# Kernel optimization log

Hardware: AMD Instinct MI355X
Metric: run time of the kernel (lower is better)

The kernel has to match this reference:

```python
import jax, jax.numpy as jnp
import numpy as np

N = 100_000          # nodes
E = 1_600_000        # edges (avg degree 16)
N_GRAPHS = 64        # batched graphs for sum_nodes readout
SLOPE_ATTN = 0.2     # leaky_relu slope on attention logits (GAT standard)
SLOPE_INTER = 0.01   # F.leaky_relu default between layers


def _gat_layer(xn, xe, src, dst, Wn, bn, Wv, bv, We, be, a_s, a_e, a_d, a_b, num_nodes):
    # Multi-head GAT with edge features. Wn:[H,Din,Dz] attn proj, Wv:[H,Din,Do] value proj,
    # We:[H,Ein,De] edge proj. Attention logit = a_s.z_src + a_e.ze + a_d.z_dst + b
    # (equivalent to attn_fc(cat(z_src, ze, z_dst)) without materializing the concat).
    z = jnp.einsum('nd,hdk->nhk', xn, Wn) + bn            # [N,H,Dz]
    v = jnp.einsum('nd,hdk->nhk', xn, Wv) + bv            # [N,H,Do]
    ze = jnp.einsum('ed,hdk->ehk', xe, We) + be           # [E,H,De]
    s = (jnp.einsum('ehk,hk->eh', z[src], a_s)
         + jnp.einsum('ehk,hk->eh', ze, a_e)
         + jnp.einsum('ehk,hk->eh', z[dst], a_d) + a_b)   # [E,H]
    s = jax.nn.leaky_relu(s, SLOPE_ATTN)
    # edge-softmax grouped by destination node (stable)
    m = jax.ops.segment_max(s, dst, num_segments=num_nodes)
    m = jnp.where(jnp.isfinite(m), m, 0.0)
    ex = jnp.exp(s - m[dst])
    den = jax.ops.segment_sum(ex, dst, num_segments=num_nodes)
    alpha = ex / (den[dst] + 1e-9)                        # [E,H]
    h = jax.ops.segment_sum(alpha[..., None] * v[src], dst, num_segments=num_nodes)  # [N,H,Do]
    Eh, H, De = ze.shape
    return h.reshape(num_nodes, -1), ze.reshape(Eh, H * De)


def setup_inputs() -> dict:
    key = jax.random.key(0)
    ks = jax.random.split(key, 32)
    f = lambda i, shape: jax.random.normal(ks[i], shape, dtype=jnp.float32) * 0.1
    return dict(
        node_types=f(0, (N, 14)),
        node_labels=f(1, (N, 50)),
        edge_labels=f(2, (E, 32)),
        src=jax.random.randint(ks[3], (E,), 0, N),
        dst=jax.random.randint(ks[4], (E,), 0, N),
        graph_ids=jnp.sort(jax.random.randint(ks[5], (N,), 0, N_GRAPHS)),
        l0_Wn=f(6, (2, 64, 32)), l0_bn=f(7, (2, 32)),
        l0_Wv=f(8, (2, 64, 64)), l0_bv=f(9, (2, 64)),
        l0_We=f(10, (2, 32, 16)), l0_be=f(11, (2, 16)),
        l0_as=f(12, (2, 32)), l0_ae=f(13, (2, 16)), l0_ad=f(14, (2, 32)), l0_ab=f(15, (2,)),
        l1_Wn=f(16, (2, 128, 32)), l1_bn=f(17, (2, 32)),
        l1_Wv=f(18, (2, 128, 64)), l1_bv=f(19, (2, 64)),
        l1_We=f(20, (2, 32, 16)), l1_be=f(21, (2, 16)),
        l1_as=f(22, (2, 32)), l1_ae=f(23, (2, 16)), l1_ad=f(24, (2, 32)), l1_ab=f(25, (2,)),
        fc_W=f(26, (128, 2)), fc_b=f(27, (2,)),
    )


def reference(node_types, node_labels, edge_labels, src, dst, graph_ids,
              l0_Wn, l0_bn, l0_Wv, l0_bv, l0_We, l0_be, l0_as, l0_ae, l0_ad, l0_ab,
              l1_Wn, l1_bn, l1_Wv, l1_bv, l1_We, l1_be, l1_as, l1_ae, l1_ad, l1_ab,
              fc_W, fc_b):
    xn = jnp.concatenate([node_types, node_labels], axis=1)   # node_features_use == 'all'
    xe = edge_labels
    xn, xe = _gat_layer(xn, xe, src, dst, l0_Wn, l0_bn, l0_Wv, l0_bv,
                        l0_We, l0_be, l0_as, l0_ae, l0_ad, l0_ab, N)
    xn = jax.nn.leaky_relu(xn, SLOPE_INTER)
    xe = jax.nn.leaky_relu(xe, SLOPE_INTER)
    xn, xe = _gat_layer(xn, xe, src, dst, l1_Wn, l1_bn, l1_Wv, l1_bv,
                        l1_We, l1_be, l1_as, l1_ae, l1_ad, l1_ab, N)
    # dgl.sum_nodes over batched graphs, then classification FC
    graph_sum = jax.ops.segment_sum(xn, graph_ids, num_segments=N_GRAPHS)  # [G, 128]
    return graph_sum @ fc_W + fc_b
```

## Files before the change

### kernel.cpp

```cpp
#include <hip/hip_runtime.h>

#define NN 100000
#define EE 1600000
#define NG 64

#define BSH 9
#define NWIN 512
#define NB 196
#define CAP 10240
#define EPB 4096

#define OFF_WS0 0
#define OFF_WD0 128
#define OFF_CS0 256
#define OFF_CD0 258
#define OFF_U1  260
#define OFF_C1  324
#define OFF_WS1 512
#define OFF_WD1 768
#define OFF_CS1 1024
#define OFF_CD1 1026
#define OFF_WT0 2048
#define FOLD_FLOATS 4096

typedef __attribute__((ext_vector_type(8))) short short8;
typedef __attribute__((ext_vector_type(4))) float f32x4;

__device__ __forceinline__ unsigned encm(float f) {
  unsigned u = __float_as_uint(f);
  return (u & 0x80000000u) ? ~u : (u | 0x80000000u);
}
__device__ __forceinline__ float decm(unsigned u) {
  return (u & 0x80000000u) ? __uint_as_float(u & 0x7FFFFFFFu) : __uint_as_float(~u);
}
__device__ __forceinline__ unsigned bf16r(float f) {
  unsigned u = __float_as_uint(f);
  return (u + 0x7FFFu + ((u >> 16) & 1u)) >> 16;
}

__global__ void fold_k(const float* __restrict__ Wn0, const float* __restrict__ bn0,
                       const float* __restrict__ as0, const float* __restrict__ ad0,
                       const float* __restrict__ We0,
                       const float* __restrict__ We1, const float* __restrict__ be1,
                       const float* __restrict__ ae1,
                       const float* __restrict__ Wn1, const float* __restrict__ bn1,
                       const float* __restrict__ as1, const float* __restrict__ ad1,
                       const float* __restrict__ Wv1,
                       float* __restrict__ fold, unsigned* __restrict__ w1tw) {
  int t = threadIdx.x;
  for (int i = t; i < 128; i += 256) {
    int h = i >> 6, d = i & 63;
    float s = 0.f, sd = 0.f;
    for (int k = 0; k < 32; ++k) {
      float w = Wn0[h*2048 + d*32 + k];
      s  += w * as0[h*32 + k];
      sd += w * ad0[h*32 + k];
    }
    fold[OFF_WS0 + i] = s; fold[OFF_WD0 + i] = sd;
  }
  for (int i = t; i < 64; i += 256) {
    int h = i >> 5, d = i & 31;
    float s = 0.f;
    for (int k = 0; k < 16; ++k) s += We1[h*512 + d*16 + k] * ae1[h*16 + k];
    fold[OFF_U1 + i] = s;
  }
  for (int i = t; i < 1024; i += 256) {
    int o = i >> 5, d = i & 31;
    fold[OFF_WT0 + o*32 + d] = We0[(o >> 4)*512 + d*16 + (o & 15)];
  }
  for (int i = t; i < 8192; i += 256) {
    int o = i >> 6, dw = i & 63;
    int d0 = 2*dw, d1 = d0 + 1;
    float f0 = Wv1[(o >> 6)*8192 + d0*64 + (o & 63)];
    float f1 = Wv1[(o >> 6)*8192 + d1*64 + (o & 63)];
    w1tw[i] = bf16r(f0) | (bf16r(f1) << 16);
  }
  if (t < 256) {
    int i = t, h = i >> 7, d = i & 127;
    float s = 0.f, sd = 0.f;
    for (int k = 0; k < 32; ++k) {
      float w = Wn1[h*4096 + d*32 + k];
      s  += w * as1[h*32 + k];
      sd += w * ad1[h*32 + k];
    }
    fold[OFF_WS1 + i] = s; fold[OFF_WD1 + i] = sd;
  }
  if (t < 2) {
    float cs = 0.f, cd = 0.f;
    for (int k = 0; k < 32; ++k) { cs += bn0[t*32+k]*as0[t*32+k]; cd += bn0[t*32+k]*ad0[t*32+k]; }
    fold[OFF_CS0 + t] = cs; fold[OFF_CD0 + t] = cd;
    float c1 = 0.f;
    for (int k = 0; k < 16; ++k) c1 += ae1[t*16+k]*be1[t*16+k];
    fold[OFF_C1 + t] = c1;
    float cs1 = 0.f, cd1 = 0.f;
    for (int k = 0; k < 32; ++k) { cs1 += bn1[t*32+k]*as1[t*32+k]; cd1 += bn1[t*32+k]*ad1[t*32+k]; }
    fold[OFF_CS1 + t] = cs1; fold[OFF_CD1 + t] = cd1;
  }
}

__global__ __launch_bounds__(256) void binA_k(const int* __restrict__ dst,
                                              int* __restrict__ bcur, uint2* __restrict__ stg) {
  __shared__ int hist[NB], gbase[NB];
  int tid = threadIdx.x;
  for (int i = tid; i < NB; i += 256) hist[i] = 0;
  __syncthreads();
  int e0 = blockIdx.x*EPB;
  int dd[16], li[16];
  #pragma unroll
  for (int q = 0; q < 16; ++q) {
    int e = e0 + q*256 + tid;
    if (e < EE) {
      int dn = dst[e];
      dd[q] = dn;
      li[q] = atomicAdd(&hist[dn >> BSH], 1);
    }
  }
  __syncthreads();
  if (tid < NB) gbase[tid] = atomicAdd(&bcur[tid], hist[tid]);
  __syncthreads();
  #pragma unroll
  for (int q = 0; q < 16; ++q) {
    int e = e0 + q*256 + tid;
    if (e < EE) {
      int b = dd[q] >> BSH;
      int idx = gbase[b] + li[q];
      if (idx < CAP) stg[(size_t)b*CAP + idx] = make_uint2((unsigned)e, (unsigned)dd[q]);
    }
  }
}

__global__ void scanB_k(const int* __restrict__ bcur, int* __restrict__ bbase) {
  int s = 0;
  for (int b = 0; b < NB; ++b) { bbase[b] = s; s += bcur[b]; }
}

__global__ __launch_bounds__(256) void binB_k(const uint2* __restrict__ stg, const int* __restrict__ bcur,
                                              const int* __restrict__ bbase,
                                              int* __restrict__ off, int* __restrict__ eid,
                                              int* __restrict__ dnp) {
  __shared__ int hist[NWIN], curx[NWIN], wsum[4];
  int tid = threadIdx.x, lane = tid & 63, w = tid >> 6;
  int b = blockIdx.x;
  int nbase = b << BSH;
  int cnt = bcur[b], base = bbase[b];
  for (int i = tid; i < NWIN; i += 256) hist[i] = 0;
  __syncthreads();
  const uint2* sp = stg + (size_t)b*CAP;
  for (int i = tid; i < cnt; i += 256) atomicAdd(&hist[sp[i].y - nbase], 1);
  __syncthreads();
  int a0 = hist[2*tid], a1 = hist[2*tid + 1];
  int tsum = a0 + a1;
  int x = tsum;
  #pragma unroll
  for (int o = 1; o < 64; o <<= 1) { int y = __shfl_up(x, o); if (lane >= o) x += y; }
  if (lane == 63) wsum[w] = x;
  __syncthreads();
  if (tid == 0) { int s = 0; for (int q = 0; q < 4; ++q) { int t = wsum[q]; wsum[q] = s; s += t; } }
  __syncthreads();
  int excl = wsum[w] + x - tsum;
  curx[2*tid]     = base + excl;
  curx[2*tid + 1] = base + excl + a0;
  __syncthreads();
  for (int j = tid; j < NWIN; j += 256) {
    int n = nbase + j;
    if (n < NN) off[n] = curx[j];
  }
  if (b == NB - 1 && tid == 0) off[NN] = base + cnt;
  __syncthreads();
  for (int i = tid; i < cnt; i += 256) {
    uint2 r = sp[i];
    int p = atomicAdd(&curx[r.y - nbase], 1);
    eid[p] = (int)r.x;
    dnp[p] = (int)r.y;
  }
}

__global__ __launch_bounds__(128) void node0v_k(const float* __restrict__ nt, const float* __restrict__ nl,
                                                const float* __restrict__ Wv0, const float* __restrict__ bv0,
                                                unsigned* __restrict__ v0b) {
  int tid = threadIdx.x;
  int h = tid >> 6, k = tid & 63;
  int sl2 = k & 31;
  float w[64];
  #pragma unroll
  for (int d = 0; d < 64; ++d) w[d] = Wv0[h*4096 + d*64 + k];
  float b = bv0[tid];
  int nb = blockIdx.x * 8;
  #pragma unroll 1
  for (int r = 0; r < 8; ++r) {
    int n = nb + r;
    const float* nrow = nt + (size_t)n*14;
    const float* lrow = nl + (size_t)n*50;
    float acc = b;
    #pragma unroll
    for (int d = 0; d < 14; ++d) acc = fmaf(nrow[d], w[d], acc);
    #pragma unroll
    for (int d = 0; d < 50; ++d) acc = fmaf(lrow[d], w[14 + d], acc);
    float p0 = __shfl(acc, 2*sl2);
    float p1 = __shfl(acc, 2*sl2 + 1);
    if (k < 32) v0b[(size_t)n*64 + h*32 + sl2] = bf16r(p0) | (bf16r(p1) << 16);
  }
}

__global__ __launch_bounds__(256) void nodez_k(const float* __restrict__ nt, const float* __restrict__ nl,
                                               const float* __restrict__ fold,
                                               float* __restrict__ zs0, float* __restrict__ zd0) {
  int n = blockIdx.x*256 + threadIdx.x;
  if (n >= NN) return;
  float p0 = 0.f, p1 = 0.f, p2 = 0.f, p3 = 0.f;
  #pragma unroll
  for (int d = 0; d < 64; ++d) {
    float x = (d < 14) ? nt[(size_t)n*14 + d] : nl[(size_t)n*50 + d - 14];
    p0 = fmaf(x, fold[OFF_WS0 + d],      p0);
    p1 = fmaf(x, fold[OFF_WS0 + 64 + d], p1);
    p2 = fmaf(x, fold[OFF_WD0 + d],      p2);
    p3 = fmaf(x, fold[OFF_WD0 + 64 + d], p3);
  }
  zs0[n*2]   = p0 + fold[OFF_CS0];
  zs0[n*2+1] = p1 + fold[OFF_CS0+1];
  zd0[n*2]   = p2 + fold[OFF_CD0];
  zd0[n*2+1] = p3 + fold[OFF_CD0+1];
}

__global__ __launch_bounds__(256) void edge0_k(const float* __restrict__ xe,
                                               const int* __restrict__ src,
                                               const int* __restrict__ eid, const int* __restrict__ dnp,
                                               const float* __restrict__ be0,
                                               const float* __restrict__ ae0, const float* __restrict__ ab0,
                                               const float* __restrict__ fold,
                                               const float* __restrict__ zs0, const float* __restrict__ zd0,
                                               float4* __restrict__ ebuf, float* __restrict__ et1p,
                                               int* __restrict__ snp,
                                               unsigned* __restrict__ menc0, unsigned* __restrict__ menc1) {
  int p = blockIdx.x*256 + threadIdx.x;
  int lane = threadIdx.x & 63;
  int e = eid[p];
  int dn = dnp[p];
  int sn = src[e];
  const float4* xp = reinterpret_cast<const float4*>(xe + (size_t)e*32);
  float4 xv[8];
  #pragma unroll
  for (int q = 0; q < 8; ++q) xv[q] = xp[q];
  const float* WT = fold + OFF_WT0;
  const float* U1 = fold + OFF_U1;
  float s0 = 0.f, s1 = 0.f, etA = 0.f, etB = 0.f;
  #pragma unroll 4
  for (int o = 0; o < 16; ++o) {
    float acc = be0[o];
    #pragma unroll
    for (int q = 0; q < 8; ++q) {
      float4 w = *reinterpret_cast<const float4*>(WT + o*32 + q*4);
      acc = fmaf(xv[q].x, w.x, acc); acc = fmaf(xv[q].y, w.y, acc);
      acc = fmaf(xv[q].z, w.z, acc); acc = fmaf(xv[q].w, w.w, acc);
    }
    s0 = fmaf(ae0[o], acc, s0);
    float lz = acc >= 0.f ? acc : 0.01f*acc;
    etA = fmaf(lz, U1[o], etA); etB = fmaf(lz, U1[32 + o], etB);
  }
  #pragma unroll 4
  for (int o = 16; o < 32; ++o) {
    float acc = be0[o];
    #pragma unroll
    for (int q = 0; q < 8; ++q) {
      float4 w = *reinterpret_cast<const float4*>(WT + o*32 + q*4);
      acc = fmaf(xv[q].x, w.x, acc); acc = fmaf(xv[q].y, w.y, acc);
      acc = fmaf(xv[q].z, w.z, acc); acc = fmaf(xv[q].w, w.w, acc);
    }
    s1 = fmaf(ae0[o], acc, s1);
    float lz = acc >= 0.f ? acc : 0.01f*acc;
    etA = fmaf(lz, U1[o], etA); etB = fmaf(lz, U1[32 + o], etB);
  }
  float2 zsv = *reinterpret_cast<const float2*>(zs0 + (size_t)sn*2);
  float2 zdv = *reinterpret_cast<const float2*>(zd0 + (size_t)dn*2);
  float l0 = zsv.x + s0 + zdv.x + ab0[0];
  float l1 = zsv.y + s1 + zdv.y + ab0[1];
  l0 = l0 >= 0.f ? l0 : 0.2f*l0;
  l1 = l1 >= 0.f ? l1 : 0.2f*l1;
  float etA1 = etA + fold[OFF_C1], etB1 = etB + fold[OFF_C1+1];
  ebuf[p] = make_float4(__int_as_float(sn), l0, l1, 0.f);
  *reinterpret_cast<float2*>(et1p + (size_t)p*2) = make_float2(etA1, etB1);
  snp[p] = sn;
  unsigned e0 = encm(l0), e1 = encm(l1), e2 = encm(etA1), e3 = encm(etB1);
  #pragma unroll
  for (int o = 1; o < 64; o <<= 1) {
    int pdn = __shfl_down(dn, o);
    unsigned q0 = __shfl_down(e0, o);
    unsigned q1 = __shfl_down(e1, o);
    unsigned q2 = __shfl_down(e2, o);
    unsigned q3 = __shfl_down(e3, o);
    if (pdn == dn) { e0 = max(e0, q0); e1 = max(e1, q1); e2 = max(e2, q2); e3 = max(e3, q3); }
  }
  int prev = __shfl_up(dn, 1);
  if (lane == 0 || prev != dn) {
    atomicMax(&menc0[(size_t)dn*2],   e0);
    atomicMax(&menc0[(size_t)dn*2+1], e1);
    atomicMax(&menc1[(size_t)dn*2],   e2);
    atomicMax(&menc1[(size_t)dn*2+1], e3);
  }
}

__global__ __launch_bounds__(256) void agg0_k(const int* __restrict__ off,
                                              const float4* __restrict__ ebuf,
                                              const unsigned* __restrict__ menc,
                                              const unsigned* __restrict__ v0b,
                                              const float* __restrict__ fold,
                                              unsigned* __restrict__ xb,
                                              float* __restrict__ zs1, float* __restrict__ zd1) {
  int tid = threadIdx.x, w = tid >> 6, lane = tid & 63;
  int n = blockIdx.x*4 + w;
  int head = lane >> 5;
  int st = off[n], en = off[n+1];
  float m = decm(menc[(size_t)n*2 + head]);
  float alo = 0.f, ahi = 0.f, den = 0.f;
  for (int i = st; i < en; i += 8) {
    int nv = en - i;
    float4 eb[8]; unsigned vr[8];
    #pragma unroll
    for (int q = 0; q < 8; ++q) if (q < nv) eb[q] = ebuf[i + q];
    #pragma unroll
    for (int q = 0; q < 8; ++q) if (q < nv) vr[q] = v0b[(size_t)__float_as_int(eb[q].x)*64 + lane];
    #pragma unroll
    for (int q = 0; q < 8; ++q) {
      if (q < nv) {
        float s = head ? eb[q].z : eb[q].y;
        float e = __expf(s - m);
        den += e;
        alo = fmaf(e, __uint_as_float(vr[q] << 16),         alo);
        ahi = fmaf(e, __uint_as_float(vr[q] & 0xFFFF0000u), ahi);
      }
    }
  }
  float inv = 1.f / (den + 1e-9f);
  float xlo = alo*inv, xhi = ahi*inv;
  xlo = xlo >= 0.f ? xlo : 0.01f*xlo;
  xhi = xhi >= 0.f ? xhi : 0.01f*xhi;
  xb[(size_t)n*64 + lane] = bf16r(xlo) | (bf16r(xhi) << 16);
  const float2* ws1 = reinterpret_cast<const float2*>(fold + OFF_WS1);
  const float2* wd1 = reinterpret_cast<const float2*>(fold + OFF_WD1);
  float2 wa = ws1[lane], wb = ws1[64 + lane], wc = wd1[lane], wd = wd1[64 + lane];
  float p0 = xlo*wa.x + xhi*wa.y;
  float p1 = xlo*wb.x + xhi*wb.y;
  float p2 = xlo*wc.x + xhi*wc.y;
  float p3 = xlo*wd.x + xhi*wd.y;
  #pragma unroll
  for (int o = 32; o > 0; o >>= 1) {
    p0 += __shfl_down(p0, o); p1 += __shfl_down(p1, o);
    p2 += __shfl_down(p2, o); p3 += __shfl_down(p3, o);
  }
  if (lane == 0) {
    zs1[n*2]   = p0 + fold[OFF_CS1];
    zs1[n*2+1] = p1 + fold[OFF_CS1+1];
    zd1[n*2]   = p2 + fold[OFF_CD1];
    zd1[n*2+1] = p3 + fold[OFF_CD1+1];
  }
}

__global__ __launch_bounds__(256) void zmax_k(const float* __restrict__ zs1, unsigned* __restrict__ zmaxenc) {
  int n = blockIdx.x*256 + threadIdx.x;
  int lane = threadIdx.x & 63;
  unsigned e0 = 0u, e1 = 0u;
  if (n < NN) {
    e0 = encm(zs1[(size_t)n*2]);
    e1 = encm(zs1[(size_t)n*2 + 1]);
  }
  #pragma unroll
  for (int o = 32; o > 0; o >>= 1) {
    e0 = max(e0, (unsigned)__shfl_down(e0, o));
    e1 = max(e1, (unsigned)__shfl_down(e1, o));
  }
  if (lane == 0) {
    atomicMax(&zmaxenc[0], e0);
    atomicMax(&zmaxenc[1], e1);
  }
}

__global__ __launch_bounds__(256) void node1m_k(const unsigned* __restrict__ xb,
                                                const unsigned* __restrict__ w1tw,
                                                const float* __restrict__ bv1,
                                                unsigned short* __restrict__ v1s) {
  int tid = threadIdx.x, w = tid >> 6, lane = tid & 63;
  int tile = blockIdx.x*4 + w;
  if (tile >= NN/16) return;
  int row = lane & 15, kg = lane >> 4;
  int n = tile*16 + row;
  short8 a[4];
  #pragma unroll
  for (int ks = 0; ks < 4; ++ks)
    a[ks] = *reinterpret_cast<const short8*>(xb + (size_t)n*64 + ks*16 + kg*4);
  #pragma unroll 2
  for (int t = 0; t < 8; ++t) {
    float bias = bv1[t*16 + row];
    f32x4 acc = {bias, bias, bias, bias};
    #pragma unroll
    for (int ks = 0; ks < 4; ++ks) {
      short8 b = *reinterpret_cast<const short8*>(w1tw + (size_t)(t*16 + row)*64 + ks*16 + kg*4);
      acc = __builtin_amdgcn_mfma_f32_16x16x32_bf16(a[ks], b, acc, 0, 0, 0);
    }
    int o = t*16 + row;
    #pragma unroll
    for (int r = 0; r < 4; ++r) {
      int nr = tile*16 + kg*4 + r;
      v1s[(size_t)nr*128 + o] = (unsigned short)bf16r(acc[r]);
    }
  }
}

__global__ void outinit_k(const float* __restrict__ fcb, float* __restrict__ out) {
  int i = threadIdx.x;
  out[i] = fcb[i & 1];
}

__global__ __launch_bounds__(256) void agg1_k(const int* __restrict__ off,
                                              const int* __restrict__ snp,
                                              const float* __restrict__ et1p,
                                              const float* __restrict__ zs1, const float* __restrict__ zd1,
                                              const float* __restrict__ ab1,
                                              const unsigned* __restrict__ menc1,
                                              const unsigned* __restrict__ zmaxenc,
                                              const unsigned* __restrict__ v1b,
                                              const float* __restrict__ fcW,
                                              float* __restrict__ pnode) {
  int tid = threadIdx.x, w = tid >> 6, lane = tid & 63;
  int n = blockIdx.x*4 + w;
  int head = lane >> 5;
  int st = off[n], en = off[n+1];
  float cnode = zd1[(size_t)n*2 + head] + ab1[head];
  float B = decm(menc1[(size_t)n*2 + head]) + decm(zmaxenc[head]) + cnode;
  float m = B >= 0.f ? B : 0.2f*B;
  float alo = 0.f, ahi = 0.f, den = 0.f;
  for (int i = st; i < en; i += 8) {
    int nv = en - i;
    int sn[8]; float et[8]; unsigned vr[8]; float zr[8];
    #pragma unroll
    for (int q = 0; q < 8; ++q) {
      if (q < nv) {
        sn[q] = snp[i + q];
        et[q] = et1p[(size_t)(i + q)*2 + head];
      }
    }
    #pragma unroll
    for (int q = 0; q < 8; ++q) {
      if (q < nv) {
        vr[q] = v1b[(size_t)sn[q]*64 + lane];
        zr[q] = zs1[(size_t)sn[q]*2 + head];
      }
    }
    #pragma unroll
    for (int q = 0; q < 8; ++q) {
      if (q < nv) {
        float l = zr[q] + et[q] + cnode;
        l = l >= 0.f ? l : 0.2f*l;
        float e = __expf(l - m);
        den += e;
        alo = fmaf(e, __uint_as_float(vr[q] << 16),         alo);
        ahi = fmaf(e, __uint_as_float(vr[q] & 0xFFFF0000u), ahi);
      }
    }
  }
  float inv = 1.f / (den + 1e-9f);
  float hlo = alo*inv, hhi = ahi*inv;
  const float2* fw2 = reinterpret_cast<const float2*>(fcW);
  float2 f0 = fw2[2*lane], f1 = fw2[2*lane + 1];
  float p0 = hlo*f0.x + hhi*f1.x;
  float p1 = hlo*f0.y + hhi*f1.y;
  #pragma unroll
  for (int o = 32; o > 0; o >>= 1) {
    p0 += __shfl_down(p0, o);
    p1 += __shfl_down(p1, o);
  }
  if (lane == 0) {
    pnode[n*2]   = p0;
    pnode[n*2+1] = p1;
  }
}

__global__ __launch_bounds__(256) void gsum_k(const float* __restrict__ pnode, const int* __restrict__ gid,
                                              float* __restrict__ out) {
  int n = blockIdx.x*256 + threadIdx.x;
  int lane = threadIdx.x & 63;
  bool ok = n < NN;
  int g = ok ? gid[n] : -1;
  float p0 = ok ? pnode[n*2]   : 0.f;
  float p1 = ok ? pnode[n*2+1] : 0.f;
  #pragma unroll
  for (int o = 1; o < 64; o <<= 1) {
    int pg = __shfl_down(g, o);
    float q0 = __shfl_down(p0, o);
    float q1 = __shfl_down(p1, o);
    if ((lane + o) < 64 && pg == g) { p0 += q0; p1 += q1; }
  }
  int prev = __shfl_up(g, 1);
  if (ok && (lane == 0 || prev != g)) {
    atomicAdd(&out[g*2],     p0);
    atomicAdd(&out[g*2 + 1], p1);
  }
}

extern "C" void kernel_launch(void* const* d_in, const int* in_sizes, int n_in,
                              void* d_out, int out_size, void* d_ws, size_t ws_size,
                              hipStream_t stream) {
  const float* nt  = (const float*)d_in[0];
  const float* nl  = (const float*)d_in[1];
  const float* xe  = (const float*)d_in[2];
  const int*   src = (const int*)d_in[3];
  const int*   dst = (const int*)d_in[4];
  const int*   gid = (const int*)d_in[5];
  const float* Wn0 = (const float*)d_in[6],  *bn0 = (const float*)d_in[7];
  const float* Wv0 = (const float*)d_in[8],  *bv0 = (const float*)d_in[9];
  const float* We0 = (const float*)d_in[10], *be0 = (const float*)d_in[11];
  const float* as0 = (const float*)d_in[12], *ae0 = (const float*)d_in[13];
  const float* ad0 = (const float*)d_in[14], *ab0 = (const float*)d_in[15];
  const float* Wn1 = (const float*)d_in[16], *bn1 = (const float*)d_in[17];
  const float* Wv1 = (const float*)d_in[18], *bv1 = (const float*)d_in[19];
  const float* We1 = (const float*)d_in[20], *be1 = (const float*)d_in[21];
  const float* as1 = (const float*)d_in[22], *ae1 = (const float*)d_in[23];
  const float* ad1 = (const float*)d_in[24], *ab1 = (const float*)d_in[25];
  const float* fcW = (const float*)d_in[26], *fcb = (const float*)d_in[27];
  float* out = (float*)d_out;

  float* fold  = (float*)d_ws;
  float* zs    = fold + FOLD_FLOATS;
  float* zd    = zs + (size_t)NN*2;
  unsigned* v0b = (unsigned*)(zd + (size_t)NN*2);
  unsigned* v1b = v0b + (size_t)NN*64;
  unsigned* xb  = v1b + (size_t)NN*64;
  unsigned* w1tw = xb + (size_t)NN*64;
  float* et1p  = (float*)(w1tw + 128*64);
  float* ebuff = et1p + (size_t)EE*2;
  unsigned* menc0 = (unsigned*)(ebuff + (size_t)EE*4);
  unsigned* menc1 = menc0 + (size_t)NN*2;
  unsigned* zmaxenc = menc1 + (size_t)NN*2;
  int* bcur   = (int*)(zmaxenc + 2);
  int* bbase  = bcur + NB;
  float* pnode = (float*)(bbase + NB);
  int* off    = (int*)(pnode + (size_t)NN*2);
  int* eid    = off + NN + 1;
  int* dnp    = eid + EE;
  int* snp    = dnp + EE;
  uint2* stg  = (uint2*)(snp + EE);
  float4* ebuf = (float4*)ebuff;

  hipMemsetAsync(menc0, 0, ((size_t)NN*4 + 2 + NB)*sizeof(unsigned), stream);
  fold_k<<<1, 256, 0, stream>>>(Wn0, bn0, as0, ad0, We0, We1, be1, ae1, Wn1, bn1, as1, ad1, Wv1, fold, w1tw);
  binA_k<<<(EE + EPB - 1)/EPB, 256, 0, stream>>>(dst, bcur, stg);
  scanB_k<<<1, 1, 0, stream>>>(bcur, bbase);
  binB_k<<<NB, 256, 0, stream>>>(stg, bcur, bbase, off, eid, dnp);
  node0v_k<<<NN/8, 128, 0, stream>>>(nt, nl, Wv0, bv0, v0b);
  nodez_k<<<(NN + 255)/256, 256, 0, stream>>>(nt, nl, fold, zs, zd);
  edge0_k<<<EE/256, 256, 0, stream>>>(xe, src, eid, dnp, be0, ae0, ab0, fold, zs, zd,
                                      ebuf, et1p, snp, menc0, menc1);
  agg0_k<<<NN/4, 256, 0, stream>>>(off, ebuf, menc0, v0b, fold, xb, zs, zd);
  zmax_k<<<(NN + 255)/256, 256, 0, stream>>>(zs, zmaxenc);
  node1m_k<<<(NN/16 + 3)/4, 256, 0, stream>>>(xb, w1tw, bv1, (unsigned short*)v1b);
  outinit_k<<<1, 128, 0, stream>>>(fcb, out);
  agg1_k<<<NN/4, 256, 0, stream>>>(off, snp, et1p, zs, zd, ab1, menc1, zmaxenc, v1b, fcW, pnode);
  gsum_k<<<(NN + 255)/256, 256, 0, stream>>>(pnode, gid, out);
}
```

Measured before the change: 589.4 us.

## Shrink edge buffer to float2 logits, reuse snp, deepen aggregation batches

```diff
diff --git a/kernel.cpp b/kernel.cpp
--- a/kernel.cpp
+++ b/kernel.cpp
@@ -229,7 +229,7 @@
                                                const float* __restrict__ ae0, const float* __restrict__ ab0,
                                                const float* __restrict__ fold,
                                                const float* __restrict__ zs0, const float* __restrict__ zd0,
-                                               float4* __restrict__ ebuf, float* __restrict__ et1p,
+                                               float* __restrict__ sbuf, float* __restrict__ et1p,
                                                int* __restrict__ snp,
                                                unsigned* __restrict__ menc0, unsigned* __restrict__ menc1) {
   int p = blockIdx.x*256 + threadIdx.x;
@@ -277,7 +277,7 @@
   l0 = l0 >= 0.f ? l0 : 0.2f*l0;
   l1 = l1 >= 0.f ? l1 : 0.2f*l1;
   float etA1 = etA + fold[OFF_C1], etB1 = etB + fold[OFF_C1+1];
-  ebuf[p] = make_float4(__int_as_float(sn), l0, l1, 0.f);
+  *reinterpret_cast<float2*>(sbuf + (size_t)p*2) = make_float2(l0, l1);
   *reinterpret_cast<float2*>(et1p + (size_t)p*2) = make_float2(etA1, etB1);
   snp[p] = sn;
   unsigned e0 = encm(l0), e1 = encm(l1), e2 = encm(etA1), e3 = encm(etB1);
@@ -300,7 +300,8 @@
 }
 
 __global__ __launch_bounds__(256) void agg0_k(const int* __restrict__ off,
-                                              const float4* __restrict__ ebuf,
+                                              const float* __restrict__ sbuf,
+                                              const int* __restrict__ snp,
                                               const unsigned* __restrict__ menc,
                                               const unsigned* __restrict__ v0b,
                                               const float* __restrict__ fold,
@@ -312,18 +313,22 @@
   int st = off[n], en = off[n+1];
   float m = decm(menc[(size_t)n*2 + head]);
   float alo = 0.f, ahi = 0.f, den = 0.f;
-  for (int i = st; i < en; i += 8) {
+  for (int i = st; i < en; i += 16) {
     int nv = en - i;
-    float4 eb[8]; unsigned vr[8];
-    #pragma unroll
-    for (int q = 0; q < 8; ++q) if (q < nv) eb[q] = ebuf[i + q];
-    #pragma unroll
-    for (int q = 0; q < 8; ++q) if (q < nv) vr[q] = v0b[(size_t)__float_as_int(eb[q].x)*64 + lane];
-    #pragma unroll
-    for (int q = 0; q < 8; ++q) {
+    int sn[16]; float lg[16]; unsigned vr[16];
+    #pragma unroll
+    for (int q = 0; q < 16; ++q) {
       if (q < nv) {
-        float s = head ? eb[q].z : eb[q].y;
-        float e = __expf(s - m);
+        sn[q] = snp[i + q];
+        lg[q] = sbuf[(size_t)(i + q)*2 + head];
+      }
+    }
+    #pragma unroll
+    for (int q = 0; q < 16; ++q) if (q < nv) vr[q] = v0b[(size_t)sn[q]*64 + lane];
+    #pragma unroll
+    for (int q = 0; q < 16; ++q) {
+      if (q < nv) {
+        float e = __expf(lg[q] - m);
         den += e;
         alo = fmaf(e, __uint_as_float(vr[q] << 16),         alo);
         ahi = fmaf(e, __uint_as_float(vr[q] & 0xFFFF0000u), ahi);
@@ -428,27 +433,27 @@
   float B = decm(menc1[(size_t)n*2 + head]) + decm(zmaxenc[head]) + cnode;
   float m = B >= 0.f ? B : 0.2f*B;
   float alo = 0.f, ahi = 0.f, den = 0.f;
-  for (int i = st; i < en; i += 8) {
+  for (int i = st; i < en; i += 16) {
     int nv = en - i;
-    int sn[8]; float et[8]; unsigned vr[8]; float zr[8];
-    #pragma unroll
-    for (int q = 0; q < 8; ++q) {
+    int sn[16]; float se[16]; unsigned vr[16];
+    #pragma unroll
+    for (int q = 0; q < 16; ++q) {
       if (q < nv) {
         sn[q] = snp[i + q];
-        et[q] = et1p[(size_t)(i + q)*2 + head];
+        se[q] = et1p[(size_t)(i + q)*2 + head];
       }
     }
     #pragma unroll
-    for (int q = 0; q < 8; ++q) {
+    for (int q = 0; q < 16; ++q) {
       if (q < nv) {
         vr[q] = v1b[(size_t)sn[q]*64 + lane];
-        zr[q] = zs1[(size_t)sn[q]*2 + head];
+        se[q] += zs1[(size_t)sn[q]*2 + head];
       }
     }
     #pragma unroll
-    for (int q = 0; q < 8; ++q) {
+    for (int q = 0; q < 16; ++q) {
       if (q < nv) {
-        float l = zr[q] + et[q] + cnode;
+        float l = se[q] + cnode;
         l = l >= 0.f ? l : 0.2f*l;
         float e = __expf(l - m);
         den += e;
@@ -526,8 +531,8 @@
   unsigned* xb  = v1b + (size_t)NN*64;
   unsigned* w1tw = xb + (size_t)NN*64;
   float* et1p  = (float*)(w1tw + 128*64);
-  float* ebuff = et1p + (size_t)EE*2;
-  unsigned* menc0 = (unsigned*)(ebuff + (size_t)EE*4);
+  float* sbuf  = et1p + (size_t)EE*2;
+  unsigned* menc0 = (unsigned*)(sbuf + (size_t)EE*2);
   unsigned* menc1 = menc0 + (size_t)NN*2;
   unsigned* zmaxenc = menc1 + (size_t)NN*2;
   int* bcur   = (int*)(zmaxenc + 2);
@@ -538,7 +543,6 @@
   int* dnp    = eid + EE;
   int* snp    = dnp + EE;
   uint2* stg  = (uint2*)(snp + EE);
-  float4* ebuf = (float4*)ebuff;
 
   hipMemsetAsync(menc0, 0, ((size_t)NN*4 + 2 + NB)*sizeof(unsigned), stream);
   fold_k<<<1, 256, 0, stream>>>(Wn0, bn0, as0, ad0, We0, We1, be1, ae1, Wn1, bn1, as1, ad1, Wv1, fold, w1tw);
@@ -548,8 +552,8 @@
   node0v_k<<<NN/8, 128, 0, stream>>>(nt, nl, Wv0, bv0, v0b);
   nodez_k<<<(NN + 255)/256, 256, 0, stream>>>(nt, nl, fold, zs, zd);
   edge0_k<<<EE/256, 256, 0, stream>>>(xe, src, eid, dnp, be0, ae0, ab0, fold, zs, zd,
-                                      ebuf, et1p, snp, menc0, menc1);
-  agg0_k<<<NN/4, 256, 0, stream>>>(off, ebuf, menc0, v0b, fold, xb, zs, zd);
+                                      sbuf, et1p, snp, menc0, menc1);
+  agg0_k<<<NN/4, 256, 0, stream>>>(off, sbuf, snp, menc0, v0b, fold, xb, zs, zd);
   zmax_k<<<(NN + 255)/256, 256, 0, stream>>>(zs, zmaxenc);
   node1m_k<<<(NN/16 + 3)/4, 256, 0, stream>>>(xb, w1tw, bv1, (unsigned short*)v1b);
   outinit_k<<<1, 128, 0, stream>>>(fcb, out);
```

After: 597.4 us. Within noise of the previous version (+1.4%).
